# Performance work log

Measured on AMD Instinct MI355X. Metric: run time of the kernel, lower is better.

Reference implementation:

```python
import jax, jax.numpy as jnp
import numpy as np

B, N_LAT, N_CTX, DIM = 4, 512, 4096, 512
HEADS, DIM_HEAD = 8, 64
DIM_INNER = HEADS * DIM_HEAD  # 512


def setup_inputs() -> dict:
    key = jax.random.key(0)
    k1, k2, k3, k4, k5 = jax.random.split(key, 5)
    x = jax.random.normal(k1, (B, N_LAT, DIM), dtype=jnp.float32)
    context = jax.random.normal(k2, (B, N_CTX, DIM), dtype=jnp.float32)
    # eqx.nn.Linear weights have shape (out_features, in_features); scale ~ 1/sqrt(in)
    s = 1.0 / np.sqrt(DIM)
    Wq = jax.random.normal(k3, (DIM_INNER, DIM), dtype=jnp.float32) * s
    Wkv = jax.random.normal(k4, (2 * DIM_INNER, DIM), dtype=jnp.float32) * s
    Wout = jax.random.normal(k5, (DIM, DIM_INNER), dtype=jnp.float32) * (1.0 / np.sqrt(DIM_INNER))
    return {"x": x, "context": context, "Wq": Wq, "Wkv": Wkv, "Wout": Wout}


def reference(x, context, Wq, Wkv, Wout):
    h, d = HEADS, DIM_HEAD
    # queries are prepended to the context (unconditional in the source)
    ctx = jnp.concatenate([x, context], axis=1)              # [b, n+m, dim]
    q = jnp.einsum('bnd,ed->bne', x, Wq)                     # [b, n, h*d]
    kv = jnp.einsum('bmd,ed->bme', ctx, Wkv)                 # [b, n+m, 2*h*d]
    k, v = jnp.split(kv, 2, axis=-1)
    # b n (h d) -> b h n d
    def split_heads(t):
        b, n, _ = t.shape
        return t.reshape(b, n, h, d).transpose(0, 2, 1, 3)
    q, k, v = split_heads(q), split_heads(k), split_heads(v)
    scale = d ** (-0.5)
    scores = jnp.einsum('bhnd,bhmd->bhnm', q, k) * scale     # [b, h, n, n+m]
    attn = jax.nn.softmax(scores, axis=-1)
    out = jnp.einsum('bhnm,bhmd->bhnd', attn, v)             # [b, h, n, d]
    b, _, n, _ = out.shape
    out = out.transpose(0, 2, 1, 3).reshape(b, n, h * d)     # b h n d -> b n (h d)
    return jnp.einsum('bne,de->bnd', out, Wout)
```

## Files before the change

kernel.cpp:

```cpp
#include <hip/hip_runtime.h>
#include <hip/hip_bf16.h>
#include <cstdint>

#define DEVI __device__ __forceinline__

typedef unsigned short u16;
typedef unsigned int u32;
typedef __attribute__((ext_vector_type(8))) short bf16x8;
typedef __attribute__((ext_vector_type(4))) float f32x4;
typedef __attribute__((ext_vector_type(4))) int i32x4;

DEVI u16 f2bf(float f) {
    union { float f; u32 u; } v; v.f = f;
    u32 r = v.u + 0x7fffu + ((v.u >> 16) & 1u);
    return (u16)(r >> 16);
}
DEVI u32 pk2(float a, float b) { return (u32)f2bf(a) | ((u32)f2bf(b) << 16); }

DEVI u32 cvtpk_bf16(float lo, float hi) {
    u32 r;
    asm("v_cvt_pk_bf16_f32 %0, %1, %2" : "=v"(r) : "v"(lo), "v"(hi));
    return r;
}

DEVI void gload_lds16(const void* g, void* l) {
    __builtin_amdgcn_global_load_lds(
        (const __attribute__((address_space(1))) u32*)(uintptr_t)g,
        (__attribute__((address_space(3))) u32*)(u32)(uintptr_t)l,
        16, 0, 0);
}


__global__ __launch_bounds__(256) void build_ctxb(const float* __restrict__ x,
                                                  const float* __restrict__ ctx,
                                                  u16* __restrict__ out) {
    int idx = blockIdx.x * 256 + threadIdx.x;
    long e0 = (long)idx * 8;
    int b = (int)(e0 / (4608L * 512));
    long rem = e0 % (4608L * 512);
    int m = (int)(rem / 512);
    int d = (int)(rem % 512);
    const float* src = (m < 512) ? (x + ((long)b * 512 + m) * 512 + d)
                                 : (ctx + ((long)b * 4096 + (m - 512)) * 512 + d);
    float4 a = *(const float4*)src;
    float4 c = *(const float4*)(src + 4);
    uint4 u;
    u.x = pk2(a.x, a.y); u.y = pk2(a.z, a.w);
    u.z = pk2(c.x, c.y); u.w = pk2(c.z, c.w);
    *(uint4*)&out[e0] = u;
}

__global__ __launch_bounds__(256) void cast_bf16(const float* __restrict__ s,
                                                 u16* __restrict__ d) {
    int i = blockIdx.x * 256 + threadIdx.x;
    const float4* s4 = (const float4*)s;
    float4 a = s4[i * 2], b = s4[i * 2 + 1];
    uint4 u;
    u.x = pk2(a.x, a.y); u.y = pk2(a.z, a.w);
    u.z = pk2(b.x, b.y); u.w = pk2(b.z, b.w);
    ((uint4*)d)[i] = u;
}

template <typename CT, bool SPLITV>
__global__ __launch_bounds__(256) void gemm_bt(const u16* __restrict__ A,
                                               const u16* __restrict__ B,
                                               CT* __restrict__ C,
                                               u16* __restrict__ VT,
                                               int N, int rpb, long bstride) {
    const int K = 512;
    __shared__ u16 Asm[2][128 * 64];
    __shared__ u16 Bsm[2][128 * 64];
    int tid = threadIdx.x;
    int w = tid >> 6, l = tid & 63;
    int g = l >> 4, c = l & 15;
    int wr = w >> 1, wc = w & 1;
    long r0 = (long)blockIdx.y * 128;
    long arow0 = (r0 / rpb) * bstride + (r0 % rpb) * K;
    int n0 = blockIdx.x * 128;

    f32x4 acc[4][4];
#pragma unroll
    for (int i = 0; i < 4; i++)
#pragma unroll
        for (int j = 0; j < 4; j++) acc[i][j] = (f32x4){0.f, 0.f, 0.f, 0.f};

    int srow = l >> 3;
    int sch = l & 7;

    auto stage = [&](int kt, int bb) {
#pragma unroll
        for (int i = 0; i < 4; i++) {
            int c2 = w * 4 + i;
            int row = c2 * 8 + srow;
            int sc = sch ^ (row & 7);
            gload_lds16(A + arow0 + (long)row * K + kt * 64 + sc * 8,
                        &Asm[bb][c2 * 512 + (l << 3)]);
            gload_lds16(B + (long)(n0 + row) * K + kt * 64 + sc * 8,
                        &Bsm[bb][c2 * 512 + (l << 3)]);
        }
    };

    stage(0, 0);
#pragma unroll 2
    for (int kt = 0; kt < 8; ++kt) {
        int pb = kt & 1;
        if (kt < 7) {
            stage(kt + 1, pb ^ 1);
            asm volatile("s_waitcnt vmcnt(8)" ::: "memory");
        } else {
            asm volatile("s_waitcnt vmcnt(0)" ::: "memory");
        }
        __builtin_amdgcn_s_barrier();
        __builtin_amdgcn_sched_barrier(0);
#pragma unroll
        for (int ks = 0; ks < 2; ++ks) {
            bf16x8 af[4], bfr[4];
#pragma unroll
            for (int mt = 0; mt < 4; ++mt) {
                int row = wr * 64 + mt * 16 + c;
                int ch = (ks * 4 + g) ^ (row & 7);
                af[mt] = *(const bf16x8*)&Asm[pb][row * 64 + ch * 8];
            }
#pragma unroll
            for (int nt = 0; nt < 4; ++nt) {
                int row = wc * 64 + nt * 16 + c;
                int ch = (ks * 4 + g) ^ (row & 7);
                bfr[nt] = *(const bf16x8*)&Bsm[pb][row * 64 + ch * 8];
            }
#pragma unroll
            for (int mt = 0; mt < 4; ++mt)
#pragma unroll
                for (int nt = 0; nt < 4; ++nt)
                    acc[mt][nt] = __builtin_amdgcn_mfma_f32_16x16x32_bf16(
                        af[mt], bfr[nt], acc[mt][nt], 0, 0, 0);
        }
        __builtin_amdgcn_s_barrier();
    }

    if constexpr (SPLITV) {
        if (n0 >= 512) {
            int b2 = (int)(r0 / rpb);
            int mb = (int)(r0 - (long)b2 * rpb) + wr * 64;
#pragma unroll
            for (int mt = 0; mt < 4; ++mt) {
#pragma unroll
                for (int nt = 0; nt < 4; ++nt) {
                    int colv = (n0 - 512) + wc * 64 + nt * 16 + c;
                    int hh = colv >> 6, dd = colv & 63;
                    long ob = ((long)(b2 * 8 + hh) * 64 + dd) * 4608 + mb + mt * 16 + g * 4;
                    ushort4 pk;
                    pk.x = f2bf(acc[mt][nt][0]);
                    pk.y = f2bf(acc[mt][nt][1]);
                    pk.z = f2bf(acc[mt][nt][2]);
                    pk.w = f2bf(acc[mt][nt][3]);
                    *(ushort4*)&VT[ob] = pk;
                }
            }
            return;
        }
    }
#pragma unroll
    for (int mt = 0; mt < 4; ++mt) {
#pragma unroll
        for (int r = 0; r < 4; ++r) {
            long row = r0 + wr * 64 + mt * 16 + g * 4 + r;
#pragma unroll
            for (int nt = 0; nt < 4; ++nt) {
                int col = n0 + wc * 64 + nt * 16 + c;
                float v = acc[mt][nt][r];
                if constexpr (sizeof(CT) == 2) {
                    C[row * (long)N + col] = (CT)f2bf(v);
                } else {
                    C[row * (long)N + col] = v;
                }
            }
        }
    }
}

__global__ __launch_bounds__(256) void attn_kern(const u16* __restrict__ Q,
                                                 const u16* __restrict__ KB,
                                                 const u16* __restrict__ VT,
                                                 float* __restrict__ Op,
                                                 float2* __restrict__ ML) {
    __shared__ u16 Ksm[2][64 * 64];
    __shared__ u16 Vsm[2][64 * 64];
    int tid = threadIdx.x;
    int w = tid >> 6, l = tid & 63;
    int g = l >> 4, c = l & 15;
    int id = blockIdx.x;
    int u = (id & 7) | ((id >> 6) << 3);
    int qi = (id >> 3) & 7;
    int p_ = u >> 2, chunk = u & 3;
    int b = p_ >> 3, h = p_ & 7;
    int qb0 = qi * 64;
    const int NT = 18;
    int it0 = chunk * NT;

    bf16x8 qf[2];
    {
        long qrow = (long)(b * 512 + qb0 + w * 16 + c);
#pragma unroll
        for (int ks = 0; ks < 2; ++ks)
            qf[ks] = *(const bf16x8*)&Q[qrow * 512 + h * 64 + ks * 32 + g * 8];
    }
    f32x4 o[4];
#pragma unroll
    for (int nt = 0; nt < 4; nt++) o[nt] = (f32x4){0.f, 0.f, 0.f, 0.f};
    float mrun = -1e30f, lrun = 0.f;

    const float SCL = 0.125f * 1.44269504f;
    int srow8 = l >> 3, sch = l & 7;
    const long kbase = (long)b * 4608 * 512 + h * 64;
    const long vtbase = (long)(b * 8 + h) * 64 * 4608;

    int g2 = g << 1;
    int srcA = ((g2 & 3) << 4) | c;
    int srcB = (((g2 | 1) & 3) << 4) | c;
    bool hiT2 = (g >> 1) != 0;

    auto stage = [&](int it, int bb) {
#pragma unroll
        for (int i = 0; i < 2; i++) {
            int c2 = w * 2 + i;
            int row = c2 * 8 + srow8;
            int sc = sch ^ (row & 7);
            gload_lds16(KB + kbase + (long)(it * 64 + row) * 512 + sc * 8,
                        &Ksm[bb][c2 * 512 + (l << 3)]);
            gload_lds16(VT + vtbase + (long)row * 4608 + it * 64 + sc * 8,
                        &Vsm[bb][c2 * 512 + (l << 3)]);
        }
    };

    stage(it0, 0);
#pragma unroll 2
    for (int t = 0; t < NT; ++t) {
        int pbuf = t & 1;
        if (t + 1 < NT) {
            stage(it0 + t + 1, pbuf ^ 1);
            asm volatile("s_waitcnt vmcnt(4)" ::: "memory");
        } else {
            asm volatile("s_waitcnt vmcnt(0)" ::: "memory");
        }
        __builtin_amdgcn_s_barrier();
        __builtin_amdgcn_sched_barrier(0);

        f32x4 st[4];
#pragma unroll
        for (int t2 = 0; t2 < 4; t2++) st[t2] = (f32x4){0.f, 0.f, 0.f, 0.f};
        __builtin_amdgcn_s_setprio(1);
#pragma unroll
        for (int ks = 0; ks < 2; ++ks) {
#pragma unroll
            for (int t2 = 0; t2 < 4; t2++) {
                int row = t2 * 16 + c;
                int ch = (ks * 4 + g) ^ (row & 7);
                bf16x8 kf = *(const bf16x8*)&Ksm[pbuf][row * 64 + ch * 8];
                st[t2] = __builtin_amdgcn_mfma_f32_16x16x32_bf16(kf, qf[ks], st[t2], 0, 0, 0);
            }
        }
        __builtin_amdgcn_s_setprio(0);

        float mx01 = fmaxf(fmaxf(st[0][0], st[0][1]), fmaxf(st[0][2], st[0][3]));
        float mx23 = fmaxf(fmaxf(st[1][0], st[1][1]), fmaxf(st[1][2], st[1][3]));
        float mx45 = fmaxf(fmaxf(st[2][0], st[2][1]), fmaxf(st[2][2], st[2][3]));
        float mx67 = fmaxf(fmaxf(st[3][0], st[3][1]), fmaxf(st[3][2], st[3][3]));
        float mx = fmaxf(fmaxf(mx01, mx23), fmaxf(mx45, mx67)) * SCL;
        mx = fmaxf(mx, __shfl_xor(mx, 16));
        mx = fmaxf(mx, __shfl_xor(mx, 32));

        bool need = mx > mrun + 8.f;
        if (__ballot(need)) {
            float mnew = fmaxf(mrun, mx);
            float rf = exp2f(mrun - mnew);
            mrun = mnew;
            lrun *= rf;
#pragma unroll
            for (int nt = 0; nt < 4; nt++)
#pragma unroll
                for (int r = 0; r < 4; r++) o[nt][r] *= rf;
        }
#pragma unroll
        for (int t2 = 0; t2 < 4; t2++)
#pragma unroll
            for (int r = 0; r < 4; r++) st[t2][r] = exp2f(st[t2][r] * SCL - mrun);

        float s01 = (st[0][0] + st[0][1]) + (st[0][2] + st[0][3]);
        float s23 = (st[1][0] + st[1][1]) + (st[1][2] + st[1][3]);
        float s45 = (st[2][0] + st[2][1]) + (st[2][2] + st[2][3]);
        float s67 = (st[3][0] + st[3][1]) + (st[3][2] + st[3][3]);
        float su = (s01 + s23) + (s45 + s67);
        su += __shfl_xor(su, 16);
        su += __shfl_xor(su, 32);
        lrun += su;

        u32 u01[4], u23[4];
#pragma unroll
        for (int t2 = 0; t2 < 4; t2++) {
            u01[t2] = cvtpk_bf16(st[t2][0], st[t2][1]);
            u23[t2] = cvtpk_bf16(st[t2][2], st[t2][3]);
        }
        bf16x8 pbf[2];
#pragma unroll
        for (int ks = 0; ks < 2; ++ks) {
            u32 a0 = (u32)__shfl((int)u01[2 * ks], srcA);
            u32 a1 = (u32)__shfl((int)u01[2 * ks + 1], srcA);
            u32 b0 = (u32)__shfl((int)u23[2 * ks], srcA);
            u32 b1 = (u32)__shfl((int)u23[2 * ks + 1], srcA);
            u32 c0 = (u32)__shfl((int)u01[2 * ks], srcB);
            u32 c1 = (u32)__shfl((int)u01[2 * ks + 1], srcB);
            u32 d0 = (u32)__shfl((int)u23[2 * ks], srcB);
            u32 d1 = (u32)__shfl((int)u23[2 * ks + 1], srcB);
            i32x4 vv;
            vv[0] = (int)(hiT2 ? a1 : a0);
            vv[1] = (int)(hiT2 ? b1 : b0);
            vv[2] = (int)(hiT2 ? c1 : c0);
            vv[3] = (int)(hiT2 ? d1 : d0);
            pbf[ks] = __builtin_bit_cast(bf16x8, vv);
        }

        __builtin_amdgcn_s_setprio(1);
#pragma unroll
        for (int ks = 0; ks < 2; ++ks) {
#pragma unroll
            for (int nt = 0; nt < 4; nt++) {
                int vrow = nt * 16 + c;
                int vch = (ks * 4 + g) ^ (vrow & 7);
                bf16x8 vb = *(const bf16x8*)&Vsm[pbuf][vrow * 64 + vch * 8];
                o[nt] = __builtin_amdgcn_mfma_f32_16x16x32_bf16(vb, pbf[ks], o[nt], 0, 0, 0);
            }
        }
        __builtin_amdgcn_s_setprio(0);
        __builtin_amdgcn_s_barrier();
    }

    long prow = (long)(chunk * 32 + p_) * 512 + qb0 + w * 16;
#pragma unroll
    for (int nt = 0; nt < 4; nt++)
        *(f32x4*)&Op[(prow + c) * 64 + nt * 16 + g * 4] = o[nt];
    if (g == 0) ML[prow + c] = make_float2(mrun, lrun);
}

__global__ __launch_bounds__(256) void attn_combine(const float* __restrict__ Op,
                                                    const float2* __restrict__ ML,
                                                    u16* __restrict__ O) {
    int tid = threadIdx.x;
    int w = tid >> 6, l = tid & 63;
    long rid = (long)blockIdx.x * 4 + w;
    int p_ = (int)(rid >> 9);
    int row = (int)(rid & 511);
    int b = p_ >> 3, h = p_ & 7;
    float2 m[4];
#pragma unroll
    for (int cc = 0; cc < 4; cc++) m[cc] = ML[((long)(cc * 32 + p_) * 512 + row)];
    float mstar = fmaxf(fmaxf(m[0].x, m[1].x), fmaxf(m[2].x, m[3].x));
    float wsum = 0.f, acc = 0.f;
#pragma unroll
    for (int cc = 0; cc < 4; cc++) {
        float wgt = exp2f(m[cc].x - mstar);
        wsum += wgt * m[cc].y;
        acc += wgt * Op[((long)(cc * 32 + p_) * 512 + row) * 64 + l];
    }
    O[((long)(b * 512 + row)) * 512 + h * 64 + l] = f2bf(acc / wsum);
}


extern "C" void kernel_launch(void* const* d_in, const int* in_sizes, int n_in,
                              void* d_out, int out_size, void* d_ws, size_t ws_size,
                              hipStream_t stream) {
    const float* x = (const float*)d_in[0];
    const float* ctx = (const float*)d_in[1];
    const float* Wq = (const float*)d_in[2];
    const float* Wkv = (const float*)d_in[3];
    const float* Wout = (const float*)d_in[4];
    float* out = (float*)d_out;

    char* ws = (char*)d_ws;
    size_t off = 0;
    auto alloc = [&](size_t bytes) {
        size_t r = off;
        off += (bytes + 255) & ~(size_t)255;
        return r;
    };
    u16* ctxb = (u16*)(ws + alloc(4L * 4608 * 512 * 2));
    u16* wqb = (u16*)(ws + alloc(512L * 512 * 2));
    u16* wkvb = (u16*)(ws + alloc(1024L * 512 * 2));
    u16* woutb = (u16*)(ws + alloc(512L * 512 * 2));
    u16* qb = (u16*)(ws + alloc(2048L * 512 * 2));
    u16* kb = (u16*)(ws + alloc(4L * 4608 * 512 * 2));
    u16* vtb = (u16*)(ws + alloc(4L * 8 * 64 * 4608 * 2));
    u16* aob = (u16*)(ws + alloc(2048L * 512 * 2));
    float* opb = (float*)(ws + alloc(4L * 32 * 512 * 64 * 4));
    float2* mlb = (float2*)(ws + alloc(4L * 32 * 512 * 8));

    build_ctxb<<<dim3(4608), dim3(256), 0, stream>>>(x, ctx, ctxb);
    cast_bf16<<<dim3(128), dim3(256), 0, stream>>>(Wq, wqb);
    cast_bf16<<<dim3(256), dim3(256), 0, stream>>>(Wkv, wkvb);
    cast_bf16<<<dim3(128), dim3(256), 0, stream>>>(Wout, woutb);

    gemm_bt<u16, false><<<dim3(4, 16), dim3(256), 0, stream>>>(
        ctxb, wqb, qb, nullptr, 512, 512, (long)4608 * 512);
    gemm_bt<u16, true><<<dim3(8, 144), dim3(256), 0, stream>>>(
        ctxb, wkvb, kb, vtb, 512, 4608, (long)4608 * 512);
    attn_kern<<<dim3(1024), dim3(256), 0, stream>>>(qb, kb, vtb, opb, mlb);
    attn_combine<<<dim3(4096), dim3(256), 0, stream>>>(opb, mlb, aob);
    gemm_bt<float, false><<<dim3(4, 16), dim3(256), 0, stream>>>(
        aob, woutb, out, nullptr, 512, 2048, (long)2048 * 512);
}
```

Baseline: 199.3 us.

## Merge prep casts into one kernel and fuse Q/KV projections with wider tiles

Folds the context build and the three weight casts into a single prep launch. It also merges the Q and KV projection GEMMs into one 512-thread kernel that uses 128x256 tiles and raises MFMA priority with setprio. The aim is to cut launch overhead and let the small Q GEMM fill idle CUs alongside the KV GEMM. In exchange, the Q part wastes blocks that return early, and the doubled LDS and threads per block may reduce occupancy.

```diff
diff --git a/kernel.cpp b/kernel.cpp
--- a/kernel.cpp
+++ b/kernel.cpp
@@ -30,29 +30,40 @@
         16, 0, 0);
 }
 
-
-__global__ __launch_bounds__(256) void build_ctxb(const float* __restrict__ x,
-                                                  const float* __restrict__ ctx,
-                                                  u16* __restrict__ out) {
-    int idx = blockIdx.x * 256 + threadIdx.x;
-    long e0 = (long)idx * 8;
-    int b = (int)(e0 / (4608L * 512));
-    long rem = e0 % (4608L * 512);
-    int m = (int)(rem / 512);
-    int d = (int)(rem % 512);
-    const float* src = (m < 512) ? (x + ((long)b * 512 + m) * 512 + d)
-                                 : (ctx + ((long)b * 4096 + (m - 512)) * 512 + d);
-    float4 a = *(const float4*)src;
-    float4 c = *(const float4*)(src + 4);
-    uint4 u;
-    u.x = pk2(a.x, a.y); u.y = pk2(a.z, a.w);
-    u.z = pk2(c.x, c.y); u.w = pk2(c.z, c.w);
-    *(uint4*)&out[e0] = u;
-}
-
-__global__ __launch_bounds__(256) void cast_bf16(const float* __restrict__ s,
-                                                 u16* __restrict__ d) {
-    int i = blockIdx.x * 256 + threadIdx.x;
+__global__ __launch_bounds__(256) void prep_all(const float* __restrict__ x,
+                                                const float* __restrict__ ctx,
+                                                const float* __restrict__ Wq,
+                                                const float* __restrict__ Wkv,
+                                                const float* __restrict__ Wout,
+                                                u16* __restrict__ ctxb,
+                                                u16* __restrict__ wqb,
+                                                u16* __restrict__ wkvb,
+                                                u16* __restrict__ woutb) {
+    int id = blockIdx.x;
+    int tid = threadIdx.x;
+    if (id < 4608) {
+        int idx = id * 256 + tid;
+        long e0 = (long)idx * 8;
+        int b = (int)(e0 / (4608L * 512));
+        long rem = e0 % (4608L * 512);
+        int m = (int)(rem / 512);
+        int d = (int)(rem % 512);
+        const float* src = (m < 512) ? (x + ((long)b * 512 + m) * 512 + d)
+                                     : (ctx + ((long)b * 4096 + (m - 512)) * 512 + d);
+        float4 a = *(const float4*)src;
+        float4 c = *(const float4*)(src + 4);
+        uint4 u;
+        u.x = pk2(a.x, a.y); u.y = pk2(a.z, a.w);
+        u.z = pk2(c.x, c.y); u.w = pk2(c.z, c.w);
+        *(uint4*)&ctxb[e0] = u;
+        return;
+    }
+    const float* s;
+    u16* d;
+    int i;
+    if (id < 4736)      { s = Wq;   d = wqb;   i = (id - 4608) * 256 + tid; }
+    else if (id < 4992) { s = Wkv;  d = wkvb;  i = (id - 4736) * 256 + tid; }
+    else                { s = Wout; d = woutb; i = (id - 4992) * 256 + tid; }
     const float4* s4 = (const float4*)s;
     float4 a = s4[i * 2], b = s4[i * 2 + 1];
     uint4 u;
@@ -61,12 +72,144 @@
     ((uint4*)d)[i] = u;
 }
 
-template <typename CT, bool SPLITV>
-__global__ __launch_bounds__(256) void gemm_bt(const u16* __restrict__ A,
-                                               const u16* __restrict__ B,
-                                               CT* __restrict__ C,
-                                               u16* __restrict__ VT,
-                                               int N, int rpb, long bstride) {
+__global__ __launch_bounds__(512) void gemm_kvq(const u16* __restrict__ ctxb,
+                                                const u16* __restrict__ wkvb,
+                                                const u16* __restrict__ wqb,
+                                                u16* __restrict__ kb,
+                                                u16* __restrict__ vtb,
+                                                u16* __restrict__ qb) {
+    const int K = 512;
+    __shared__ u16 Asm[2][128 * 64];
+    __shared__ u16 Bsm[2][256 * 64];
+    int tid = threadIdx.x;
+    int w = tid >> 6, l = tid & 63;
+    int g = l >> 4, c = l & 15;
+    int wr = w >> 2, wc = w & 3;
+
+    const u16* B;
+    u16* C;
+    long r0, arow0;
+    int rpb;
+    bool isq = (blockIdx.y >= 144);
+    if (isq) {
+        if (blockIdx.x >= 2) return;
+        r0 = (long)(blockIdx.y - 144) * 128;
+        rpb = 512;
+        B = wqb;
+        C = qb;
+    } else {
+        r0 = (long)blockIdx.y * 128;
+        rpb = 4608;
+        B = wkvb;
+        C = kb;
+    }
+    arow0 = (r0 / rpb) * (4608L * 512) + (r0 % rpb) * K;
+    int n0 = blockIdx.x * 256;
+
+    f32x4 acc[4][4];
+#pragma unroll
+    for (int i = 0; i < 4; i++)
+#pragma unroll
+        for (int j = 0; j < 4; j++) acc[i][j] = (f32x4){0.f, 0.f, 0.f, 0.f};
+
+    int srow = l >> 3;
+    int sch = l & 7;
+
+    auto stage = [&](int kt, int bb) {
+#pragma unroll
+        for (int i = 0; i < 2; i++) {
+            int c2 = w * 2 + i;
+            int row = c2 * 8 + srow;
+            int sc = sch ^ (row & 7);
+            gload_lds16(ctxb + arow0 + (long)row * K + kt * 64 + sc * 8,
+                        &Asm[bb][c2 * 512 + (l << 3)]);
+        }
+#pragma unroll
+        for (int i = 0; i < 4; i++) {
+            int c2 = w * 4 + i;
+            int row = c2 * 8 + srow;
+            int sc = sch ^ (row & 7);
+            gload_lds16(B + (long)(n0 + row) * K + kt * 64 + sc * 8,
+                        &Bsm[bb][c2 * 512 + (l << 3)]);
+        }
+    };
+
+    stage(0, 0);
+#pragma unroll 2
+    for (int kt = 0; kt < 8; ++kt) {
+        int pb = kt & 1;
+        if (kt < 7) {
+            stage(kt + 1, pb ^ 1);
+            asm volatile("s_waitcnt vmcnt(6)" ::: "memory");
+        } else {
+            asm volatile("s_waitcnt vmcnt(0)" ::: "memory");
+        }
+        __builtin_amdgcn_s_barrier();
+        __builtin_amdgcn_sched_barrier(0);
+#pragma unroll
+        for (int ks = 0; ks < 2; ++ks) {
+            bf16x8 af[4], bfr[4];
+#pragma unroll
+            for (int mt = 0; mt < 4; ++mt) {
+                int row = wr * 64 + mt * 16 + c;
+                int ch = (ks * 4 + g) ^ (row & 7);
+                af[mt] = *(const bf16x8*)&Asm[pb][row * 64 + ch * 8];
+            }
+#pragma unroll
+            for (int nt = 0; nt < 4; ++nt) {
+                int row = wc * 64 + nt * 16 + c;
+                int ch = (ks * 4 + g) ^ (row & 7);
+                bfr[nt] = *(const bf16x8*)&Bsm[pb][row * 64 + ch * 8];
+            }
+            __builtin_amdgcn_s_setprio(1);
+#pragma unroll
+            for (int mt = 0; mt < 4; ++mt)
+#pragma unroll
+                for (int nt = 0; nt < 4; ++nt)
+                    acc[mt][nt] = __builtin_amdgcn_mfma_f32_16x16x32_bf16(
+                        af[mt], bfr[nt], acc[mt][nt], 0, 0, 0);
+            __builtin_amdgcn_s_setprio(0);
+        }
+        __builtin_amdgcn_s_barrier();
+    }
+
+    if (!isq && n0 >= 512) {
+        int b2 = (int)(r0 / 4608);
+        int mb = (int)(r0 - (long)b2 * 4608) + wr * 64;
+#pragma unroll
+        for (int mt = 0; mt < 4; ++mt) {
+#pragma unroll
+            for (int nt = 0; nt < 4; ++nt) {
+                int colv = (n0 - 512) + wc * 64 + nt * 16 + c;
+                int hh = colv >> 6, dd = colv & 63;
+                long ob = ((long)(b2 * 8 + hh) * 64 + dd) * 4608 + mb + mt * 16 + g * 4;
+                ushort4 pk;
+                pk.x = f2bf(acc[mt][nt][0]);
+                pk.y = f2bf(acc[mt][nt][1]);
+                pk.z = f2bf(acc[mt][nt][2]);
+                pk.w = f2bf(acc[mt][nt][3]);
+                *(ushort4*)&vtb[ob] = pk;
+            }
+        }
+        return;
+    }
+#pragma unroll
+    for (int mt = 0; mt < 4; ++mt) {
+#pragma unroll
+        for (int r = 0; r < 4; ++r) {
+            long row = r0 + wr * 64 + mt * 16 + g * 4 + r;
+#pragma unroll
+            for (int nt = 0; nt < 4; ++nt) {
+                int col = n0 + wc * 64 + nt * 16 + c;
+                C[row * 512 + col] = f2bf(acc[mt][nt][r]);
+            }
+        }
+    }
+}
+
+__global__ __launch_bounds__(256) void gemm_out(const u16* __restrict__ A,
+                                                const u16* __restrict__ B,
+                                                float* __restrict__ C) {
     const int K = 512;
     __shared__ u16 Asm[2][128 * 64];
     __shared__ u16 Bsm[2][128 * 64];
@@ -75,7 +218,7 @@
     int g = l >> 4, c = l & 15;
     int wr = w >> 1, wc = w & 1;
     long r0 = (long)blockIdx.y * 128;
-    long arow0 = (r0 / rpb) * bstride + (r0 % rpb) * K;
+    long arow0 = r0 * K;
     int n0 = blockIdx.x * 128;
 
     f32x4 acc[4][4];
@@ -136,29 +279,6 @@
         }
         __builtin_amdgcn_s_barrier();
     }
-
-    if constexpr (SPLITV) {
-        if (n0 >= 512) {
-            int b2 = (int)(r0 / rpb);
-            int mb = (int)(r0 - (long)b2 * rpb) + wr * 64;
-#pragma unroll
-            for (int mt = 0; mt < 4; ++mt) {
-#pragma unroll
-                for (int nt = 0; nt < 4; ++nt) {
-                    int colv = (n0 - 512) + wc * 64 + nt * 16 + c;
-                    int hh = colv >> 6, dd = colv & 63;
-                    long ob = ((long)(b2 * 8 + hh) * 64 + dd) * 4608 + mb + mt * 16 + g * 4;
-                    ushort4 pk;
-                    pk.x = f2bf(acc[mt][nt][0]);
-                    pk.y = f2bf(acc[mt][nt][1]);
-                    pk.z = f2bf(acc[mt][nt][2]);
-                    pk.w = f2bf(acc[mt][nt][3]);
-                    *(ushort4*)&VT[ob] = pk;
-                }
-            }
-            return;
-        }
-    }
 #pragma unroll
     for (int mt = 0; mt < 4; ++mt) {
 #pragma unroll
@@ -167,12 +287,7 @@
 #pragma unroll
             for (int nt = 0; nt < 4; ++nt) {
                 int col = n0 + wc * 64 + nt * 16 + c;
-                float v = acc[mt][nt][r];
-                if constexpr (sizeof(CT) == 2) {
-                    C[row * (long)N + col] = (CT)f2bf(v);
-                } else {
-                    C[row * (long)N + col] = v;
-                }
+                C[row * 512 + col] = acc[mt][nt][r];
             }
         }
     }
@@ -393,17 +508,10 @@
     float* opb = (float*)(ws + alloc(4L * 32 * 512 * 64 * 4));
     float2* mlb = (float2*)(ws + alloc(4L * 32 * 512 * 8));
 
-    build_ctxb<<<dim3(4608), dim3(256), 0, stream>>>(x, ctx, ctxb);
-    cast_bf16<<<dim3(128), dim3(256), 0, stream>>>(Wq, wqb);
-    cast_bf16<<<dim3(256), dim3(256), 0, stream>>>(Wkv, wkvb);
-    cast_bf16<<<dim3(128), dim3(256), 0, stream>>>(Wout, woutb);
-
-    gemm_bt<u16, false><<<dim3(4, 16), dim3(256), 0, stream>>>(
-        ctxb, wqb, qb, nullptr, 512, 512, (long)4608 * 512);
-    gemm_bt<u16, true><<<dim3(8, 144), dim3(256), 0, stream>>>(
-        ctxb, wkvb, kb, vtb, 512, 4608, (long)4608 * 512);
+    prep_all<<<dim3(5120), dim3(256), 0, stream>>>(x, ctx, Wq, Wkv, Wout,
+                                                   ctxb, wqb, wkvb, woutb);
+    gemm_kvq<<<dim3(4, 160), dim3(512), 0, stream>>>(ctxb, wkvb, wqb, kb, vtb, qb);
     attn_kern<<<dim3(1024), dim3(256), 0, stream>>>(qb, kb, vtb, opb, mlb);
     attn_combine<<<dim3(4096), dim3(256), 0, stream>>>(opb, mlb, aob);
-    gemm_bt<float, false><<<dim3(4, 16), dim3(256), 0, stream>>>(
-        aob, woutb, out, nullptr, 512, 2048, (long)2048 * 512);
-}
+    gemm_out<<<dim3(4, 16), dim3(256), 0, stream>>>(aob, woutb, out);
+}
```

After: 189.6 us. -4.9%, faster.
